# Optimization experiments

Measured on AMD Instinct MI355X. Metric: run time of the kernel, lower is better.

## Reference

```python
import jax, jax.numpy as jnp
import numpy as np

B, L, DIM, H, HD = 2, 2048, 1024, 16, 64


def _rope_tables(L, hd):
    inv_freq = 1.0 / (10000.0 ** (np.arange(0, hd, 2, dtype=np.float32) / hd))
    t = np.arange(L, dtype=np.float32)
    freqs = np.outer(t, inv_freq)                 # [L, hd/2]
    emb = np.concatenate([freqs, freqs], axis=-1)  # [L, hd]
    return jnp.asarray(np.cos(emb)), jnp.asarray(np.sin(emb))


def setup_inputs() -> dict:
    key = jax.random.key(0)
    k1, k2, k3 = jax.random.split(key, 3)
    x = jax.random.normal(k1, (B, L, DIM), dtype=jnp.float32)
    cos, sin = _rope_tables(L, HD)
    w_qkv = jax.random.normal(k2, (DIM, 3 * H * HD), dtype=jnp.float32) * (DIM ** -0.5)
    w_out = jax.random.normal(k3, (H * HD, DIM), dtype=jnp.float32) * ((H * HD) ** -0.5)
    return {"x": x, "cos": cos, "sin": sin, "w_qkv": w_qkv, "w_out": w_out}


def _rotate_half(u):
    u1, u2 = jnp.split(u, 2, axis=-1)
    return jnp.concatenate([-u2, u1], axis=-1)


def _apply_rope(u, cos, sin):
    # u: [B, L, H, hd]; cos/sin: [L, hd]
    c = cos[None, :, None, :]
    s = sin[None, :, None, :]
    return u * c + _rotate_half(u) * s


def reference(x, cos, sin, w_qkv, w_out):
    b, l, _ = x.shape
    qkv = jnp.einsum('bld,de->ble', x, w_qkv).reshape(b, l, 3 * H, HD)
    q, k, v = jnp.split(qkv, 3, axis=2)          # each [B, L, H, hd]
    q = _apply_rope(q, cos, sin)
    k = _apply_rope(k, cos, sin)
    scale = HD ** -0.5                            # SDPA default scale
    scores = jnp.einsum('bqhd,bkhd->bhqk', q, k) * scale
    attn = jax.nn.softmax(scores, axis=-1)
    o = jnp.einsum('bhqk,bkhd->bqhd', attn, v).reshape(b, l, H * HD)
    return jnp.einsum('ble,ed->bld', o, w_out)
```

## Files before the change

kernel.cpp:

```cpp
#include <hip/hip_runtime.h>
#include <hip/hip_bf16.h>

#define BATCH 2
#define SEQ   2048
#define DIM   1024
#define NH    16
#define HD    64
#define K_DIM 1024

typedef __attribute__((ext_vector_type(8))) short short8;
typedef __attribute__((ext_vector_type(4))) short short4v;
typedef __attribute__((ext_vector_type(4))) float f32x4;
typedef unsigned short ushort_t;

__device__ __forceinline__ unsigned short f2b(float x) {
    unsigned int u = __float_as_uint(x);
    u += 0x7FFFu + ((u >> 16) & 1u);
    return (unsigned short)(u >> 16);
}

#define ASYNC_COPY16(gp, lp) \
    __builtin_amdgcn_global_load_lds((const __attribute__((address_space(1))) void*)(gp), \
                                     (__attribute__((address_space(3))) void*)(lp), 16, 0, 0)

__global__ __launch_bounds__(256)
void prep(const float* __restrict__ x, const float* __restrict__ w_qkv,
          const float* __restrict__ w_out, ushort_t* __restrict__ xb,
          ushort_t* __restrict__ wqb, ushort_t* __restrict__ wob)
{
    const int bid = blockIdx.x;
    if (bid < 1024) {
        constexpr int n4 = (BATCH * SEQ * DIM) / 4;
        int i = bid * 256 + threadIdx.x;
        for (; i < n4; i += 1024 * 256) {
            float4 v = ((const float4*)x)[i];
            short4v o;
            o[0] = (short)f2b(v.x); o[1] = (short)f2b(v.y);
            o[2] = (short)f2b(v.z); o[3] = (short)f2b(v.w);
            ((short4v*)xb)[i] = o;
        }
    } else {
        const int lane = threadIdx.x & 63;
        const float* src; ushort_t* dst; int N, job;
        if (bid < 2560) { src = w_qkv; dst = wqb; N = 3072; job = (bid - 1024) * 4 + (threadIdx.x >> 6); }
        else            { src = w_out; dst = wob; N = 1024; job = (bid - 2560) * 4 + (threadIdx.x >> 6); }
        const int jn = (N == 3072) ? (job % 48) : (job % 16);
        const int jk = (N == 3072) ? (job / 48) : (job / 16);
        const int n  = jn * 64 + lane;
        const int k0 = jk * 8;
        short8 o;
        #pragma unroll
        for (int j = 0; j < 8; ++j) o[j] = (short)f2b(src[(size_t)(k0 + j) * N + n]);
        *(short8*)(dst + (size_t)n * K_DIM + k0) = o;
    }
}

__device__ __forceinline__ void gemm_stage(const ushort_t* __restrict__ Ag,
                                           const ushort_t* __restrict__ Bg,
                                           ushort_t* As, ushort_t* Bs,
                                           int k0, int w, int r0, int c0)
{
    ASYNC_COPY16(Ag + (size_t)r0 * K_DIM + k0 + c0 * 8,        As + w * 512);
    ASYNC_COPY16(Ag + (size_t)(64 + r0) * K_DIM + k0 + c0 * 8, As + w * 512 + 2048);
    ASYNC_COPY16(Bg + (size_t)r0 * K_DIM + k0 + c0 * 8,        Bs + w * 512);
    ASYNC_COPY16(Bg + (size_t)(64 + r0) * K_DIM + k0 + c0 * 8, Bs + w * 512 + 2048);
}

__device__ __forceinline__ void mfma_gemm_tile(
    const ushort_t* __restrict__ Ag, const ushort_t* __restrict__ Bg,
    ushort_t (&As)[2][128 * 32], ushort_t (&Bs)[2][128 * 32], f32x4 acc[4][4])
{
    const int t = threadIdx.x;
    const int w = t >> 6, lane = t & 63;
    const int qd = lane >> 4, cl = lane & 15;
    const int p0 = w * 64 + lane;
    const int r0 = p0 >> 2;
    const int c0 = (p0 & 3) ^ (r0 & 3);

    gemm_stage(Ag, Bg, As[0], Bs[0], 0, w, r0, c0);

    for (int kt = 0; kt < K_DIM / 32; ++kt) {
        const int cur = kt & 1;
        __syncthreads();
        if (kt + 1 < K_DIM / 32)
            gemm_stage(Ag, Bg, As[cur ^ 1], Bs[cur ^ 1], (kt + 1) * 32, w, r0, c0);

        short8 af[4], bfr[4];
        #pragma unroll
        for (int rt = 0; rt < 4; ++rt) {
            const int row = (w >> 1) * 64 + rt * 16 + cl;
            af[rt] = *(const short8*)(As[cur] + row * 32 + ((qd ^ (row & 3)) * 8));
        }
        #pragma unroll
        for (int ct = 0; ct < 4; ++ct) {
            const int col = (w & 1) * 64 + ct * 16 + cl;
            bfr[ct] = *(const short8*)(Bs[cur] + col * 32 + ((qd ^ (col & 3)) * 8));
        }
        #pragma unroll
        for (int rt = 0; rt < 4; ++rt)
            #pragma unroll
            for (int ct = 0; ct < 4; ++ct)
                acc[rt][ct] = __builtin_amdgcn_mfma_f32_16x16x32_bf16(
                    af[rt], bfr[ct], acc[rt][ct], 0, 0, 0);
    }
}

__global__ __launch_bounds__(256, 3)
void gemm_qkv_mfma(const ushort_t* __restrict__ xb, const ushort_t* __restrict__ wqb,
                   ushort_t* __restrict__ qb, ushort_t* __restrict__ kb,
                   ushort_t* __restrict__ vt,
                   const float* __restrict__ cosb, const float* __restrict__ sinb)
{
    __shared__ __align__(16) ushort_t As[2][128 * 32];
    __shared__ __align__(16) ushort_t Bs[2][128 * 32];
    const int m0 = blockIdx.y * 128, n0 = blockIdx.x * 128;

    f32x4 acc[4][4];
    #pragma unroll
    for (int i = 0; i < 4; ++i)
        #pragma unroll
        for (int j = 0; j < 4; ++j)
            #pragma unroll
            for (int r = 0; r < 4; ++r) acc[i][j][r] = 0.f;

    mfma_gemm_tile(xb + (size_t)m0 * K_DIM, wqb + (size_t)n0 * K_DIM, As, Bs, acc);

    const int t = threadIdx.x, w = t >> 6, lane = t & 63;
    const int qd = lane >> 4, cl = lane & 15;
    const int b = m0 >> 11;
    const int lbase = (m0 & 2047) + (w >> 1) * 64;
    const int region = blockIdx.x >> 3;
    const int h = (blockIdx.x & 7) * 2 + (w & 1);

    if (region < 2) {
        ushort_t* dst = region ? kb : qb;
        const float sc = region ? 1.0f : 0.18033688011111234f;
        #pragma unroll
        for (int rt = 0; rt < 4; ++rt) {
            #pragma unroll
            for (int r = 0; r < 4; ++r) {
                const int l = lbase + rt * 16 + qd * 4 + r;
                const float c0 = cosb[l * HD + cl],      s0 = sinb[l * HD + cl];
                const float c1 = cosb[l * HD + 16 + cl], s1 = sinb[l * HD + 16 + cl];
                const float v0 = acc[rt][0][r] * c0 - acc[rt][2][r] * s0;
                const float v1 = acc[rt][1][r] * c1 - acc[rt][3][r] * s1;
                const float v2 = acc[rt][2][r] * c0 + acc[rt][0][r] * s0;
                const float v3 = acc[rt][3][r] * c1 + acc[rt][1][r] * s1;
                short4v o4;
                o4[0] = (short)f2b(v0 * sc);
                o4[1] = (short)f2b(v1 * sc);
                o4[2] = (short)f2b(v2 * sc);
                o4[3] = (short)f2b(v3 * sc);
                *(short4v*)(dst + (((size_t)b * NH + h) * SEQ + l) * HD + cl * 4) = o4;
            }
        }
    } else {
        #pragma unroll
        for (int rt = 0; rt < 4; ++rt)
            #pragma unroll
            for (int ct = 0; ct < 4; ++ct) {
                const int d = ct * 16 + cl;
                const int l = lbase + rt * 16 + qd * 4;
                short4v o4;
                #pragma unroll
                for (int r = 0; r < 4; ++r) o4[r] = (short)f2b(acc[rt][ct][r]);
                *(short4v*)(vt + (((size_t)b * NH + h) * HD + d) * SEQ + l) = o4;
            }
    }
}

__device__ __forceinline__ void go_stage(const ushort_t* __restrict__ Ag,
                                         const ushort_t* __restrict__ Bg,
                                         ushort_t* As, ushort_t* Bs,
                                         int k0, int w, int lane)
{
    #pragma unroll
    for (int j = 0; j < 2; ++j) {
        const int r = w * 32 + j * 16 + (lane >> 2);
        const int c = (lane & 3) ^ (r & 3);
        ASYNC_COPY16(Ag + (size_t)r * K_DIM + k0 + c * 8, As + (w * 128 + j * 64) * 8);
    }
    const int rb = w * 16 + (lane >> 2);
    const int cb = (lane & 3) ^ (rb & 3);
    ASYNC_COPY16(Bg + (size_t)rb * K_DIM + k0 + cb * 8, Bs + (w * 64) * 8);
}

__global__ __launch_bounds__(256, 3)
void gemm_out_mfma(const ushort_t* __restrict__ ob, const ushort_t* __restrict__ wob,
                   float* __restrict__ out)
{
    __shared__ __align__(16) ushort_t As[2][128 * 32];
    __shared__ __align__(16) ushort_t Bs[2][64 * 32];
    const int m0 = blockIdx.y * 128, n0 = blockIdx.x * 64;
    const int t = threadIdx.x;
    const int w = t >> 6, lane = t & 63;
    const int qd = lane >> 4, cl = lane & 15;
    const int wr = w >> 1, wc = w & 1;

    f32x4 acc[4][2];
    #pragma unroll
    for (int i = 0; i < 4; ++i)
        #pragma unroll
        for (int j = 0; j < 2; ++j)
            #pragma unroll
            for (int r = 0; r < 4; ++r) acc[i][j][r] = 0.f;

    const ushort_t* Ag = ob  + (size_t)m0 * K_DIM;
    const ushort_t* Bg = wob + (size_t)n0 * K_DIM;
    go_stage(Ag, Bg, As[0], Bs[0], 0, w, lane);

    for (int kt = 0; kt < K_DIM / 32; ++kt) {
        const int cur = kt & 1;
        __syncthreads();
        if (kt + 1 < K_DIM / 32)
            go_stage(Ag, Bg, As[cur ^ 1], Bs[cur ^ 1], (kt + 1) * 32, w, lane);

        short8 af[4], bfr[2];
        #pragma unroll
        for (int rt = 0; rt < 4; ++rt) {
            const int row = wr * 64 + rt * 16 + cl;
            af[rt] = *(const short8*)(As[cur] + row * 32 + ((qd ^ (row & 3)) * 8));
        }
        #pragma unroll
        for (int ct = 0; ct < 2; ++ct) {
            const int col = wc * 32 + ct * 16 + cl;
            bfr[ct] = *(const short8*)(Bs[cur] + col * 32 + ((qd ^ (col & 3)) * 8));
        }
        #pragma unroll
        for (int rt = 0; rt < 4; ++rt)
            #pragma unroll
            for (int ct = 0; ct < 2; ++ct)
                acc[rt][ct] = __builtin_amdgcn_mfma_f32_16x16x32_bf16(
                    af[rt], bfr[ct], acc[rt][ct], 0, 0, 0);
    }

    const int mbase = m0 + wr * 64, nbase = n0 + wc * 32;
    #pragma unroll
    for (int rt = 0; rt < 4; ++rt)
        #pragma unroll
        for (int ct = 0; ct < 2; ++ct)
            #pragma unroll
            for (int r = 0; r < 4; ++r)
                out[(size_t)(mbase + rt * 16 + qd * 4 + r) * DIM + nbase + ct * 16 + cl] =
                    acc[rt][ct][r];
}

__global__ __launch_bounds__(256, 3)
void attn_mfma(const ushort_t* __restrict__ qb, const ushort_t* __restrict__ kb,
               const ushort_t* __restrict__ vt, float* __restrict__ Op,
               float* __restrict__ lp)
{
    const int h = blockIdx.x;
    const int b = blockIdx.y >> 1;
    const int half = blockIdx.y & 1;
    const int qt = blockIdx.z;
    const int t = threadIdx.x;
    const int w = t >> 6, lane = t & 63;
    const int qd = lane >> 4, cl = lane & 15;
    constexpr int NT = SEQ / 64 / 2;

    __shared__ __align__(16) ushort_t Ks[2][64 * 64];
    __shared__ __align__(16) ushort_t Vs[2][64 * 64];
    __shared__ __align__(16) ushort_t P[4][2048];
    char* Pb = (char*)P[w];

    const size_t bh = (size_t)b * NH + h;
    const ushort_t* qbase = qb + (bh * SEQ + qt * 128 + w * 32) * HD;
    const ushort_t* kbase = kb + bh * SEQ * HD;
    const ushort_t* vbase = vt + bh * (size_t)HD * SEQ;

    const int p0 = w * 128 + lane;
    const int r0a = p0 >> 3,  c0a = (p0 & 7) ^ (r0a & 7);
    const int p1 = p0 + 64;
    const int r1a = p1 >> 3,  c1a = (p1 & 7) ^ (r1a & 7);
    const int ldsoff0 = (w * 128) * 8;
    const int ldsoff1 = (w * 128 + 64) * 8;

    short8 qf[2][2];
    #pragma unroll
    for (int nt = 0; nt < 2; ++nt)
        #pragma unroll
        for (int kh = 0; kh < 2; ++kh)
            qf[nt][kh] = *(const short8*)(qbase + (nt * 16 + cl) * HD + kh * 32 + qd * 8);

    f32x4 oaccT[4][2];
    float l_part[2] = {0.f, 0.f};
    #pragma unroll
    for (int dt = 0; dt < 4; ++dt)
        #pragma unroll
        for (int nt = 0; nt < 2; ++nt)
            #pragma unroll
            for (int r = 0; r < 4; ++r) oaccT[dt][nt][r] = 0.f;

    short8 pf_prev[2][2], vf_prev[4][2];
    #pragma unroll
    for (int nt = 0; nt < 2; ++nt)
        #pragma unroll
        for (int kh = 0; kh < 2; ++kh)
            #pragma unroll
            for (int e = 0; e < 8; ++e) pf_prev[nt][kh][e] = 0;
    #pragma unroll
    for (int dt = 0; dt < 4; ++dt)
        #pragma unroll
        for (int kh = 0; kh < 2; ++kh)
            #pragma unroll
            for (int e = 0; e < 8; ++e) vf_prev[dt][kh][e] = 0;

    const int g0 = half * NT;
    {
        ASYNC_COPY16(kbase + (size_t)(g0 * 64 + r0a) * HD + c0a * 8, (ushort_t*)Ks[0] + ldsoff0);
        ASYNC_COPY16(kbase + (size_t)(g0 * 64 + r1a) * HD + c1a * 8, (ushort_t*)Ks[0] + ldsoff1);
        ASYNC_COPY16(vbase + (size_t)r0a * SEQ + g0 * 64 + c0a * 8,  (ushort_t*)Vs[0] + ldsoff0);
        ASYNC_COPY16(vbase + (size_t)r1a * SEQ + g0 * 64 + c1a * 8,  (ushort_t*)Vs[0] + ldsoff1);
    }

    for (int kt = 0; kt < NT; ++kt) {
        const int cur = kt & 1;
        __syncthreads();
        if (kt + 1 < NT) {
            const int g = g0 + kt + 1;
            ASYNC_COPY16(kbase + (size_t)(g * 64 + r0a) * HD + c0a * 8, (ushort_t*)Ks[cur ^ 1] + ldsoff0);
            ASYNC_COPY16(kbase + (size_t)(g * 64 + r1a) * HD + c1a * 8, (ushort_t*)Ks[cur ^ 1] + ldsoff1);
            ASYNC_COPY16(vbase + (size_t)r0a * SEQ + g * 64 + c0a * 8,  (ushort_t*)Vs[cur ^ 1] + ldsoff0);
            ASYNC_COPY16(vbase + (size_t)r1a * SEQ + g * 64 + c1a * 8,  (ushort_t*)Vs[cur ^ 1] + ldsoff1);
        }

        short8 kf[4][2], vf[4][2];
        #pragma unroll
        for (int mt = 0; mt < 4; ++mt)
            #pragma unroll
            for (int kh = 0; kh < 2; ++kh)
                kf[mt][kh] = *(const short8*)(Ks[cur] + ((mt * 16 + cl) * 8 + ((kh * 4 + qd) ^ (cl & 7))) * 8);
        #pragma unroll
        for (int dt = 0; dt < 4; ++dt)
            #pragma unroll
            for (int kh = 0; kh < 2; ++kh)
                vf[dt][kh] = *(const short8*)(Vs[cur] + ((dt * 16 + cl) * 8 + ((kh * 4 + qd) ^ (cl & 7))) * 8);

        f32x4 s[4][2];
        #pragma unroll
        for (int mt = 0; mt < 4; ++mt)
            #pragma unroll
            for (int nt = 0; nt < 2; ++nt)
                #pragma unroll
                for (int r = 0; r < 4; ++r) s[mt][nt][r] = 0.f;
        #pragma unroll
        for (int kh = 0; kh < 2; ++kh)
            #pragma unroll
            for (int mt = 0; mt < 4; ++mt)
                #pragma unroll
                for (int nt = 0; nt < 2; ++nt)
                    s[mt][nt] = __builtin_amdgcn_mfma_f32_16x16x32_bf16(
                        kf[mt][kh], qf[nt][kh], s[mt][nt], 0, 0, 0);

        #pragma unroll
        for (int kh = 0; kh < 2; ++kh)
            #pragma unroll
            for (int dt = 0; dt < 4; ++dt)
                #pragma unroll
                for (int nt = 0; nt < 2; ++nt)
                    oaccT[dt][nt] = __builtin_amdgcn_mfma_f32_16x16x32_bf16(
                        vf_prev[dt][kh], pf_prev[nt][kh], oaccT[dt][nt], 0, 0, 0);

        #pragma unroll
        for (int nt = 0; nt < 2; ++nt) {
            #pragma unroll
            for (int mt = 0; mt < 4; ++mt) {
                const float e0 = __builtin_amdgcn_exp2f(s[mt][nt][0]);
                const float e1 = __builtin_amdgcn_exp2f(s[mt][nt][1]);
                const float e2 = __builtin_amdgcn_exp2f(s[mt][nt][2]);
                const float e3 = __builtin_amdgcn_exp2f(s[mt][nt][3]);
                l_part[nt] += (e0 + e1) + (e2 + e3);
                union { __hip_bfloat162 h2[2]; unsigned long long u64; } pk;
                pk.h2[0] = __float22bfloat162_rn(make_float2(e0, e1));
                pk.h2[1] = __float22bfloat162_rn(make_float2(e2, e3));
                const int g = (mt * 2 + (qd >> 1)) ^ (cl & 7);
                *(unsigned long long*)(Pb + (nt * 16 + cl) * 128 + g * 16 + (qd & 1) * 8) = pk.u64;
            }
        }
        __builtin_amdgcn_wave_barrier();

        #pragma unroll
        for (int nt = 0; nt < 2; ++nt)
            #pragma unroll
            for (int kh = 0; kh < 2; ++kh)
                pf_prev[nt][kh] = *(const short8*)(Pb + (nt * 16 + cl) * 128 + (((kh * 4 + qd) ^ (cl & 7)) * 16));
        #pragma unroll
        for (int dt = 0; dt < 4; ++dt)
            #pragma unroll
            for (int kh = 0; kh < 2; ++kh)
                vf_prev[dt][kh] = vf[dt][kh];
    }

    #pragma unroll
    for (int kh = 0; kh < 2; ++kh)
        #pragma unroll
        for (int dt = 0; dt < 4; ++dt)
            #pragma unroll
            for (int nt = 0; nt < 2; ++nt)
                oaccT[dt][nt] = __builtin_amdgcn_mfma_f32_16x16x32_bf16(
                    vf_prev[dt][kh], pf_prev[nt][kh], oaccT[dt][nt], 0, 0, 0);

    #pragma unroll
    for (int nt = 0; nt < 2; ++nt) {
        float l = l_part[nt];
        l += __shfl_xor(l, 16);
        l += __shfl_xor(l, 32);
        const int query = qt * 128 + w * 32 + nt * 16 + cl;
        if (qd == 0)
            lp[((size_t)half * BATCH + b) * NH * SEQ + (size_t)h * SEQ + query] = l;
        float* op = Op + (((size_t)half * BATCH + b) * SEQ + query) * DIM + h * HD;
        #pragma unroll
        for (int dt = 0; dt < 4; ++dt)
            *(f32x4*)(op + dt * 16 + qd * 4) = oaccT[dt][nt];
    }
}

__global__ __launch_bounds__(256)
void reduce_o(const float* __restrict__ Op, const float* __restrict__ lp,
              ushort_t* __restrict__ ob)
{
    const int idx = blockIdx.x * 256 + threadIdx.x;
    const int d4 = idx & 255;
    const int l  = (idx >> 8) & 2047;
    const int b  = idx >> 19;
    const int h  = d4 >> 4;

    const size_t o_off = ((size_t)b * SEQ + l) * DIM + d4 * 4;
    const float4 a = *(const float4*)(Op + o_off);
    const float4 c = *(const float4*)(Op + (size_t)BATCH * SEQ * DIM + o_off);
    const size_t l_off = ((size_t)b * NH + h) * SEQ + l;
    const float inv = 1.0f / (lp[l_off] + lp[(size_t)BATCH * NH * SEQ + l_off]);

    short4v o4;
    o4[0] = (short)f2b((a.x + c.x) * inv);
    o4[1] = (short)f2b((a.y + c.y) * inv);
    o4[2] = (short)f2b((a.z + c.z) * inv);
    o4[3] = (short)f2b((a.w + c.w) * inv);
    *(short4v*)(ob + o_off) = o4;
}

extern "C" void kernel_launch(void* const* d_in, const int* in_sizes, int n_in,
                              void* d_out, int out_size, void* d_ws, size_t ws_size,
                              hipStream_t stream)
{
    const float* x     = (const float*)d_in[0];
    const float* cosb  = (const float*)d_in[1];
    const float* sinb  = (const float*)d_in[2];
    const float* w_qkv = (const float*)d_in[3];
    const float* w_out = (const float*)d_in[4];
    float* out = (float*)d_out;

    constexpr size_t MB = 1u << 20;
    char* ws = (char*)d_ws;
    ushort_t* qb  = (ushort_t*)(ws);
    ushort_t* kb  = (ushort_t*)(ws + 8 * MB);
    ushort_t* vt  = (ushort_t*)(ws + 16 * MB);
    ushort_t* wob = (ushort_t*)(ws + 24 * MB);
    float*    lp  = (float*)   (ws + 26 * MB);
    float*    Op  = (float*)   (ws + 27 * MB);
    ushort_t* xb  = (ushort_t*)(ws + 27 * MB);
    ushort_t* wqb = (ushort_t*)(ws + 35 * MB);
    ushort_t* ob  = qb;

    prep<<<3072, 256, 0, stream>>>(x, w_qkv, w_out, xb, wqb, wob);
    gemm_qkv_mfma<<<dim3(24, 32), 256, 0, stream>>>(xb, wqb, qb, kb, vt, cosb, sinb);
    attn_mfma<<<dim3(16, 4, 16), 256, 0, stream>>>(qb, kb, vt, Op, lp);
    reduce_o<<<4096, 256, 0, stream>>>(Op, lp, ob);
    gemm_out_mfma<<<dim3(16, 32), 256, 0, stream>>>(ob, wob, out);
}
```

Measured before the change: 208.3 us.

## Drop split-KV attention and fuse normalization into attention epilogue

Each attention block now walks the full key sequence instead of half of it. The softmax denominator is applied in the epilogue, which writes bf16 output directly and removes the separate reduce_o kernel. This eliminates writing and re-reading the fp32 partial outputs and denominators, plus one kernel launch. In exchange the grid shrinks to half as many blocks, each doing twice the serial work, which lowers available parallelism on the GPU. The output buffer moves to its own workspace region because the Q buffer is still being read.

```diff
diff --git a/kernel.cpp b/kernel.cpp
--- a/kernel.cpp
+++ b/kernel.cpp
@@ -247,17 +247,15 @@
 
 __global__ __launch_bounds__(256, 3)
 void attn_mfma(const ushort_t* __restrict__ qb, const ushort_t* __restrict__ kb,
-               const ushort_t* __restrict__ vt, float* __restrict__ Op,
-               float* __restrict__ lp)
+               const ushort_t* __restrict__ vt, ushort_t* __restrict__ ob)
 {
     const int h = blockIdx.x;
-    const int b = blockIdx.y >> 1;
-    const int half = blockIdx.y & 1;
+    const int b = blockIdx.y;
     const int qt = blockIdx.z;
     const int t = threadIdx.x;
     const int w = t >> 6, lane = t & 63;
     const int qd = lane >> 4, cl = lane & 15;
-    constexpr int NT = SEQ / 64 / 2;
+    constexpr int NT = SEQ / 64;
 
     __shared__ __align__(16) ushort_t Ks[2][64 * 64];
     __shared__ __align__(16) ushort_t Vs[2][64 * 64];
@@ -306,19 +304,18 @@
             #pragma unroll
             for (int e = 0; e < 8; ++e) vf_prev[dt][kh][e] = 0;
 
-    const int g0 = half * NT;
     {
-        ASYNC_COPY16(kbase + (size_t)(g0 * 64 + r0a) * HD + c0a * 8, (ushort_t*)Ks[0] + ldsoff0);
-        ASYNC_COPY16(kbase + (size_t)(g0 * 64 + r1a) * HD + c1a * 8, (ushort_t*)Ks[0] + ldsoff1);
-        ASYNC_COPY16(vbase + (size_t)r0a * SEQ + g0 * 64 + c0a * 8,  (ushort_t*)Vs[0] + ldsoff0);
-        ASYNC_COPY16(vbase + (size_t)r1a * SEQ + g0 * 64 + c1a * 8,  (ushort_t*)Vs[0] + ldsoff1);
+        ASYNC_COPY16(kbase + (size_t)r0a * HD + c0a * 8,            (ushort_t*)Ks[0] + ldsoff0);
+        ASYNC_COPY16(kbase + (size_t)r1a * HD + c1a * 8,            (ushort_t*)Ks[0] + ldsoff1);
+        ASYNC_COPY16(vbase + (size_t)r0a * SEQ + c0a * 8,           (ushort_t*)Vs[0] + ldsoff0);
+        ASYNC_COPY16(vbase + (size_t)r1a * SEQ + c1a * 8,           (ushort_t*)Vs[0] + ldsoff1);
     }
 
     for (int kt = 0; kt < NT; ++kt) {
         const int cur = kt & 1;
         __syncthreads();
         if (kt + 1 < NT) {
-            const int g = g0 + kt + 1;
+            const int g = kt + 1;
             ASYNC_COPY16(kbase + (size_t)(g * 64 + r0a) * HD + c0a * 8, (ushort_t*)Ks[cur ^ 1] + ldsoff0);
             ASYNC_COPY16(kbase + (size_t)(g * 64 + r1a) * HD + c1a * 8, (ushort_t*)Ks[cur ^ 1] + ldsoff1);
             ASYNC_COPY16(vbase + (size_t)r0a * SEQ + g * 64 + c0a * 8,  (ushort_t*)Vs[cur ^ 1] + ldsoff0);
@@ -406,38 +403,17 @@
         float l = l_part[nt];
         l += __shfl_xor(l, 16);
         l += __shfl_xor(l, 32);
+        const float inv = 1.0f / l;
         const int query = qt * 128 + w * 32 + nt * 16 + cl;
-        if (qd == 0)
-            lp[((size_t)half * BATCH + b) * NH * SEQ + (size_t)h * SEQ + query] = l;
-        float* op = Op + (((size_t)half * BATCH + b) * SEQ + query) * DIM + h * HD;
-        #pragma unroll
-        for (int dt = 0; dt < 4; ++dt)
-            *(f32x4*)(op + dt * 16 + qd * 4) = oaccT[dt][nt];
-    }
-}
-
-__global__ __launch_bounds__(256)
-void reduce_o(const float* __restrict__ Op, const float* __restrict__ lp,
-              ushort_t* __restrict__ ob)
-{
-    const int idx = blockIdx.x * 256 + threadIdx.x;
-    const int d4 = idx & 255;
-    const int l  = (idx >> 8) & 2047;
-    const int b  = idx >> 19;
-    const int h  = d4 >> 4;
-
-    const size_t o_off = ((size_t)b * SEQ + l) * DIM + d4 * 4;
-    const float4 a = *(const float4*)(Op + o_off);
-    const float4 c = *(const float4*)(Op + (size_t)BATCH * SEQ * DIM + o_off);
-    const size_t l_off = ((size_t)b * NH + h) * SEQ + l;
-    const float inv = 1.0f / (lp[l_off] + lp[(size_t)BATCH * NH * SEQ + l_off]);
-
-    short4v o4;
-    o4[0] = (short)f2b((a.x + c.x) * inv);
-    o4[1] = (short)f2b((a.y + c.y) * inv);
-    o4[2] = (short)f2b((a.z + c.z) * inv);
-    o4[3] = (short)f2b((a.w + c.w) * inv);
-    *(short4v*)(ob + o_off) = o4;
+        ushort_t* op = ob + ((size_t)b * SEQ + query) * DIM + h * HD;
+        #pragma unroll
+        for (int dt = 0; dt < 4; ++dt) {
+            short4v o4;
+            #pragma unroll
+            for (int r = 0; r < 4; ++r) o4[r] = (short)f2b(oaccT[dt][nt][r] * inv);
+            *(short4v*)(op + dt * 16 + qd * 4) = o4;
+        }
+    }
 }
 
 extern "C" void kernel_launch(void* const* d_in, const int* in_sizes, int n_in,
@@ -457,15 +433,12 @@
     ushort_t* kb  = (ushort_t*)(ws + 8 * MB);
     ushort_t* vt  = (ushort_t*)(ws + 16 * MB);
     ushort_t* wob = (ushort_t*)(ws + 24 * MB);
-    float*    lp  = (float*)   (ws + 26 * MB);
-    float*    Op  = (float*)   (ws + 27 * MB);
-    ushort_t* xb  = (ushort_t*)(ws + 27 * MB);
-    ushort_t* wqb = (ushort_t*)(ws + 35 * MB);
-    ushort_t* ob  = qb;
+    ushort_t* ob  = (ushort_t*)(ws + 26 * MB);
+    ushort_t* xb  = (ushort_t*)(ws + 34 * MB);
+    ushort_t* wqb = (ushort_t*)(ws + 42 * MB);
 
     prep<<<3072, 256, 0, stream>>>(x, w_qkv, w_out, xb, wqb, wob);
     gemm_qkv_mfma<<<dim3(24, 32), 256, 0, stream>>>(xb, wqb, qb, kb, vt, cosb, sinb);
-    attn_mfma<<<dim3(16, 4, 16), 256, 0, stream>>>(qb, kb, vt, Op, lp);
-    reduce_o<<<4096, 256, 0, stream>>>(Op, lp, ob);
+    attn_mfma<<<dim3(16, 2, 16), 256, 0, stream>>>(qb, kb, vt, ob);
     gemm_out_mfma<<<dim3(16, 32), 256, 0, stream>>>(ob, wob, out);
 }
```

Measured after the change: 205.4 us. Within noise of the previous version (-1.4%).
